# Optimization experiments

Hardware: AMD Instinct MI355X
Metric: run time of the kernel (lower is better)

## Reference

```python
import jax, jax.numpy as jnp
import numpy as np

B, V, H = 4, 256, 128
EPS = 1e-5


def setup_inputs() -> dict:
    key = jax.random.key(0)
    ks = jax.random.split(key, 16)
    s = 1.0 / np.sqrt(H)
    d = {}
    d["h"] = jax.random.normal(ks[0], (B, V, H), jnp.float32)
    d["e"] = jax.random.normal(ks[1], (B, V, V, H), jnp.float32)
    d["A"] = jax.random.bernoulli(ks[2], 0.5, (B, V, V))
    d["S"] = jax.random.bernoulli(ks[3], 0.5, (B, V, V))
    for i, n in enumerate("UVABC"):
        d["W" + n] = (jax.random.normal(ks[4 + i], (H, H), jnp.float32) * s)
        d["b" + n] = jnp.zeros((H,), jnp.float32)
    d["gamma_h"] = jnp.ones((H,), jnp.float32)
    d["beta_h"] = jnp.zeros((H,), jnp.float32)
    d["gamma_e"] = jnp.ones((H,), jnp.float32)
    d["beta_e"] = jnp.zeros((H,), jnp.float32)
    return d


def _batchnorm(x2d, gamma, beta):
    # BatchNorm1d with batch statistics (track_running_stats=False), biased var
    m = x2d.mean(axis=0)
    v = x2d.var(axis=0)
    return (x2d - m) * jax.lax.rsqrt(v + EPS) * gamma + beta


def reference(h, e, A, S, WU, bU, WV, bV, WA, bA, WB, bB, WC, bC,
              gamma_h, beta_h, gamma_e, beta_e):
    b, v, hd = h.shape
    h_in, e_in = h, e

    Uh = h @ WU.T + bU                      # (B,V,H)
    Vh = h @ WV.T + bV                      # (B,V,H)
    Ah = h @ WA.T + bA
    Bh = h @ WB.T + bB
    Ce = e @ WC.T + bC                      # (B,V,V,H)

    # e_new[b,i,j] = Ah[b,j] + Bh[b,i] + Ce[b,i,j]
    e_new = Ah[:, None, :, :] + Bh[:, :, None, :] + Ce
    gates = jax.nn.sigmoid(e_new)

    # aggregate(Vh, S, gates): zero where S is True, then sum over j
    Vh_b = Vh[:, None, :, :]                # (B,1,V,H) -> neighbor j features
    agg_S = jnp.sum(jnp.where(S[..., None], 0.0, gates * Vh_b), axis=2)
    # aggregate(Vh, A, gates=1): sum_j (1 - A[i,j]) * Vh[j] as a matmul
    agg_A = jnp.einsum('bij,bjh->bih', (~A).astype(Vh.dtype), Vh)

    h_new = Uh + agg_S + agg_A

    h_new = _batchnorm(h_new.reshape(b * v, hd), gamma_h, beta_h).reshape(b, v, hd)
    e_new = _batchnorm(e_new.reshape(b * v * v, hd), gamma_e, beta_e).reshape(b, v, v, hd)

    h_out = h_in + jax.nn.relu(h_new)
    e_out = e_in + jax.nn.relu(e_new)
    return (h_out, e_out)
```

## Files before the change

kernel.cpp:

```cpp
#include <hip/hip_runtime.h>

#define BB 4
#define VV 256
#define HH 128
#define NROWS (BB*VV)
#define NE_CNT (BB*VV*VV)
#define EPSV 1e-5f

typedef float4 f4;

__device__ __forceinline__ float sigm(float x) {
    return 1.f / (1.f + __expf(-x));
}

#define COMP(v,kk) ((kk)==0 ? (v).x : (kk)==1 ? (v).y : (kk)==2 ? (v).z : (v).w)

#define GLOAD_LDS16(g, l) __builtin_amdgcn_global_load_lds( \
    (const __attribute__((address_space(1))) unsigned int*)(g), \
    (__attribute__((address_space(3))) unsigned int*)(l), 16, 0, 0)

__global__ __launch_bounds__(256) void k_linear4(
    const float* __restrict__ h,
    const float* __restrict__ W0, const float* __restrict__ b0,
    const float* __restrict__ W1, const float* __restrict__ b1,
    const float* __restrict__ W2, const float* __restrict__ b2,
    const float* __restrict__ W3, const float* __restrict__ b3,
    float* __restrict__ out)
{
    __shared__ float hs[4*HH];
    const int tid = threadIdx.x;
    const int r0  = blockIdx.x * 4;
    if (tid < 128) {
        int r = tid >> 5, kq = (tid & 31) << 2;
        *(f4*)&hs[r*HH + kq] = *(const f4*)&h[(r0 + r)*HH + kq];
    }
    __syncthreads();
    const int n  = tid & 127;
    const int s0 = tid >> 7;
    const float* Ws[4] = {W0, W1, W2, W3};
    const float* bs[4] = {b0, b1, b2, b3};
    for (int ss = 0; ss < 2; ++ss) {
        const int sel = s0 + ss*2;
        const float* wrow = Ws[sel] + n*HH;
        float a0=0.f, a1=0.f, a2=0.f, a3=0.f;
        for (int kq = 0; kq < 32; ++kq) {
            f4 w = *(const f4*)&wrow[kq<<2];
            float wq[4] = {w.x, w.y, w.z, w.w};
            #pragma unroll
            for (int q = 0; q < 4; ++q) {
                int k = (kq<<2) + q;
                float wv = wq[q];
                a0 += hs[0*HH + k] * wv;
                a1 += hs[1*HH + k] * wv;
                a2 += hs[2*HH + k] * wv;
                a3 += hs[3*HH + k] * wv;
            }
        }
        float bias = bs[sel][n];
        float* o = out + sel*(NROWS*HH);
        o[(r0+0)*HH + n] = a0 + bias;
        o[(r0+1)*HH + n] = a1 + bias;
        o[(r0+2)*HH + n] = a2 + bias;
        o[(r0+3)*HH + n] = a3 + bias;
    }
}

__global__ __launch_bounds__(256) void k_transpose(
    const float* __restrict__ in, float* __restrict__ out)
{
    __shared__ float t[32][33];
    int ti = blockIdx.x >> 2, tj = blockIdx.x & 3;
    int tx = threadIdx.x & 31, ty = threadIdx.x >> 5;
    for (int yy = ty; yy < 32; yy += 8)
        t[yy][tx] = in[(ti*32 + yy)*HH + tj*32 + tx];
    __syncthreads();
    for (int yy = ty; yy < 32; yy += 8)
        out[(tj*32 + yy)*HH + ti*32 + tx] = t[tx][yy];
}

__global__ __launch_bounds__(256, 2) void k_edge(
    const float* __restrict__ e, const int* __restrict__ A, const int* __restrict__ S,
    const float* __restrict__ WCt, const float* __restrict__ bC,
    const float* __restrict__ Ahw, const float* __restrict__ Bhw,
    const float* __restrict__ Vhw,
    float* __restrict__ eout, float* __restrict__ aggS, float* __restrict__ aggA,
    float* __restrict__ sums)
{
    __shared__ float es[2][2048];
    __shared__ float wc[2][2048];
    __shared__ float s_aggS[HH], s_aggA[HH], s_sum[HH], s_ssq[HH];

    const int t     = threadIdx.x;
    const int bi    = blockIdx.x >> 1;
    const int jbase = (blockIdx.x & 1) << 7;
    const int b     = bi >> 8;
    if (t < HH) { s_aggS[t]=0.f; s_aggA[t]=0.f; s_sum[t]=0.f; s_ssq[t]=0.f; }

    const int tn  = t & 15;
    const int tjg = t >> 4;

    float acc[8][8];
    #pragma unroll
    for (int jj = 0; jj < 8; ++jj)
        #pragma unroll
        for (int q = 0; q < 8; ++q) acc[jj][q] = 0.f;

    const f4* e4   = (const f4*)e;
    const f4* wct4 = (const f4*)WCt;

    const int j0 = t >> 2;
    const int sp = (t & 3) ^ (j0 & 3);
    const f4* p_es0 = e4 + ((size_t)(bi*VV + jbase) + j0)*32 + sp;
    const f4* p_es1 = p_es0 + (size_t)64*32;
    const f4* p_wc  = wct4 + t;

    const int wave = t >> 6;
    const int wofs = wave * 256;

    #define STAGE(buf, kc_) do {                                        \
        float* esb_ = es[buf];                                          \
        float* wcb_ = wc[buf];                                          \
        GLOAD_LDS16(p_es0 + (kc_)*4,        &esb_[wofs]);               \
        GLOAD_LDS16(p_es1 + (kc_)*4,        &esb_[1024 + wofs]);        \
        GLOAD_LDS16(p_wc  + (kc_)*512,      &wcb_[wofs]);               \
        GLOAD_LDS16(p_wc  + (kc_)*512+256,  &wcb_[1024 + wofs]);        \
    } while (0)

    STAGE(0, 0);
    __syncthreads();

    for (int kc = 0; kc < 8; ++kc) {
        float* esb = es[kc & 1];
        float* wcb = wc[kc & 1];
        if (kc < 7) STAGE((kc & 1) ^ 1, kc + 1);
        #pragma unroll
        for (int kq = 0; kq < 4; ++kq) {
            const int sw = ((kq ^ (tjg & 3)) << 2);
            #pragma unroll
            for (int jh = 0; jh < 2; ++jh) {
                f4 a0 = *(const f4*)&esb[(tjg + (jh*4+0)*16)*16 + sw];
                f4 a1 = *(const f4*)&esb[(tjg + (jh*4+1)*16)*16 + sw];
                f4 a2 = *(const f4*)&esb[(tjg + (jh*4+2)*16)*16 + sw];
                f4 a3 = *(const f4*)&esb[(tjg + (jh*4+3)*16)*16 + sw];
                #pragma unroll
                for (int kk = 0; kk < 4; ++kk) {
                    const float* wrow = &wcb[(kq*4 + kk)*128 + tn*4];
                    f4 w0 = *(const f4*)&wrow[0];
                    f4 w1 = *(const f4*)&wrow[64];
                    float v0 = COMP(a0,kk), v1 = COMP(a1,kk);
                    float v2 = COMP(a2,kk), v3 = COMP(a3,kk);
                    #pragma unroll
                    for (int jl = 0; jl < 4; ++jl) {
                        float a = (jl==0)?v0:(jl==1)?v1:(jl==2)?v2:v3;
                        acc[jh*4+jl][0] += a*w0.x;
                        acc[jh*4+jl][1] += a*w0.y;
                        acc[jh*4+jl][2] += a*w0.z;
                        acc[jh*4+jl][3] += a*w0.w;
                        acc[jh*4+jl][4] += a*w1.x;
                        acc[jh*4+jl][5] += a*w1.y;
                        acc[jh*4+jl][6] += a*w1.z;
                        acc[jh*4+jl][7] += a*w1.w;
                    }
                }
            }
        }
        __syncthreads();
    }
    #undef STAGE

    float bcv[8], bhv[8];
    #pragma unroll
    for (int q = 0; q < 2; ++q) {
        f4 bc4 = *(const f4*)&bC[tn*4 + q*64];
        f4 bh4 = *(const f4*)&Bhw[bi*HH + tn*4 + q*64];
        bcv[q*4+0]=bc4.x; bcv[q*4+1]=bc4.y; bcv[q*4+2]=bc4.z; bcv[q*4+3]=bc4.w;
        bhv[q*4+0]=bh4.x; bhv[q*4+1]=bh4.y; bhv[q*4+2]=bh4.z; bhv[q*4+3]=bh4.w;
    }
    float sm[8], sq[8], aS[8], aA[8];
    #pragma unroll
    for (int q = 0; q < 8; ++q) { sm[q]=0.f; sq[q]=0.f; aS[q]=0.f; aA[q]=0.f; }

    const int* Sp = S + bi*VV + jbase;
    const int* Ap = A + bi*VV + jbase;
    #pragma unroll
    for (int jj = 0; jj < 8; ++jj) {
        const int j = tjg + jj*16;
        const int jg = jbase + j;
        const float* ahp = &Ahw[(size_t)(b*VV + jg)*HH];
        const float* vhp = &Vhw[(size_t)(b*VV + jg)*HH];
        const int Sij = Sp[j], Aij = Ap[j];
        #pragma unroll
        for (int q = 0; q < 2; ++q) {
            f4 ah = *(const f4*)&ahp[tn*4 + q*64];
            f4 vh = *(const f4*)&vhp[tn*4 + q*64];
            f4 env;
            env.x = acc[jj][q*4+0] + bcv[q*4+0] + bhv[q*4+0] + ah.x;
            env.y = acc[jj][q*4+1] + bcv[q*4+1] + bhv[q*4+1] + ah.y;
            env.z = acc[jj][q*4+2] + bcv[q*4+2] + bhv[q*4+2] + ah.z;
            env.w = acc[jj][q*4+3] + bcv[q*4+3] + bhv[q*4+3] + ah.w;
            *(f4*)&eout[((size_t)(bi*VV) + jg)*HH + tn*4 + q*64] = env;
            float vv[4] = {vh.x, vh.y, vh.z, vh.w};
            float ev[4] = {env.x, env.y, env.z, env.w};
            #pragma unroll
            for (int qq = 0; qq < 4; ++qq) {
                float v = ev[qq];
                sm[q*4+qq] += v;
                sq[q*4+qq] += v*v;
                if (!Aij) aA[q*4+qq] += vv[qq];
                if (!Sij) aS[q*4+qq] += vv[qq] * sigm(v);
            }
        }
    }
    #pragma unroll
    for (int q = 0; q < 2; ++q)
        #pragma unroll
        for (int qq = 0; qq < 4; ++qq) {
            int n = tn*4 + q*64 + qq;
            atomicAdd(&s_sum[n],  sm[q*4+qq]);
            atomicAdd(&s_ssq[n],  sq[q*4+qq]);
            atomicAdd(&s_aggS[n], aS[q*4+qq]);
            atomicAdd(&s_aggA[n], aA[q*4+qq]);
        }
    __syncthreads();
    if (t < HH) {
        atomicAdd(&aggS[bi*HH + t], s_aggS[t]);
        atomicAdd(&aggA[bi*HH + t], s_aggA[t]);
        atomicAdd(&sums[t],      s_sum[t]);
        atomicAdd(&sums[HH + t], s_ssq[t]);
    }
}

__global__ __launch_bounds__(256) void k_hnew(
    const float* __restrict__ Uh, const float* __restrict__ aggS,
    const float* __restrict__ aggA, float* __restrict__ h_new,
    float* __restrict__ sums)
{
    __shared__ float ssm[HH], ssq[HH];
    const int tid = threadIdx.x;
    if (tid < 128) { ssm[tid]=0.f; ssq[tid]=0.f; }
    __syncthreads();
    int gid = blockIdx.x*256 + tid;
    f4 u = *(const f4*)&Uh[gid*4];
    f4 s = *(const f4*)&aggS[gid*4];
    f4 a = *(const f4*)&aggA[gid*4];
    float v0=u.x+s.x+a.x, v1=u.y+s.y+a.y, v2=u.z+s.z+a.z, v3=u.w+s.w+a.w;
    *(f4*)&h_new[gid*4] = make_float4(v0,v1,v2,v3);
    int n0 = (gid*4) & 127;
    atomicAdd(&ssm[n0+0], v0); atomicAdd(&ssq[n0+0], v0*v0);
    atomicAdd(&ssm[n0+1], v1); atomicAdd(&ssq[n0+1], v1*v1);
    atomicAdd(&ssm[n0+2], v2); atomicAdd(&ssq[n0+2], v2*v2);
    atomicAdd(&ssm[n0+3], v3); atomicAdd(&ssq[n0+3], v3*v3);
    __syncthreads();
    if (tid < 128) {
        atomicAdd(&sums[256 + tid], ssm[tid]);
        atomicAdd(&sums[384 + tid], ssq[tid]);
    }
}

__global__ void k_stats(const float* __restrict__ sums, float* __restrict__ outs,
                        const float* __restrict__ gamma_e, const float* __restrict__ beta_e,
                        const float* __restrict__ gamma_h, const float* __restrict__ beta_h)
{
    int n = threadIdx.x;
    float em  = sums[n] * (1.f/(float)NE_CNT);
    float ev  = sums[128+n] * (1.f/(float)NE_CNT) - em*em;
    float esc = rsqrtf(ev + EPSV) * gamma_e[n];
    outs[n]       = esc;
    outs[128 + n] = beta_e[n] - em*esc;
    float hm  = sums[256+n] * (1.f/1024.f);
    float hv  = sums[384+n] * (1.f/1024.f) - hm*hm;
    float hsc = rsqrtf(hv + EPSV) * gamma_h[n];
    outs[256 + n] = hsc;
    outs[384 + n] = beta_h[n] - hm*hsc;
}

__global__ __launch_bounds__(256) void k_hout(
    const float* __restrict__ h_in, const float* __restrict__ h_new,
    const float* __restrict__ outs, float* __restrict__ hout)
{
    int gid = blockIdx.x*256 + threadIdx.x;
    int n0 = (gid*4) & 127;
    f4 x  = *(const f4*)&h_new[gid*4];
    f4 hi = *(const f4*)&h_in[gid*4];
    f4 sc = *(const f4*)&outs[256 + n0];
    f4 sh = *(const f4*)&outs[384 + n0];
    f4 y;
    y.x = fmaxf(x.x*sc.x + sh.x, 0.f) + hi.x;
    y.y = fmaxf(x.y*sc.y + sh.y, 0.f) + hi.y;
    y.z = fmaxf(x.z*sc.z + sh.z, 0.f) + hi.z;
    y.w = fmaxf(x.w*sc.w + sh.w, 0.f) + hi.w;
    *(f4*)&hout[gid*4] = y;
}

__global__ __launch_bounds__(256) void k_eout(
    const float* __restrict__ e_in, const float* __restrict__ outs,
    float* __restrict__ eio)
{
    size_t gid = (size_t)blockIdx.x*256 + threadIdx.x;
    int n0 = ((int)(gid & 31)) << 2;
    f4 x  = *(const f4*)&eio[gid*4];
    f4 ei = *(const f4*)&e_in[gid*4];
    f4 sc = *(const f4*)&outs[n0];
    f4 sh = *(const f4*)&outs[128 + n0];
    f4 y;
    y.x = fmaxf(x.x*sc.x + sh.x, 0.f) + ei.x;
    y.y = fmaxf(x.y*sc.y + sh.y, 0.f) + ei.y;
    y.z = fmaxf(x.z*sc.z + sh.z, 0.f) + ei.z;
    y.w = fmaxf(x.w*sc.w + sh.w, 0.f) + ei.w;
    *(f4*)&eio[gid*4] = y;
}

extern "C" void kernel_launch(void* const* d_in, const int* in_sizes, int n_in,
                              void* d_out, int out_size, void* d_ws, size_t ws_size,
                              hipStream_t stream)
{
    (void)in_sizes; (void)n_in; (void)out_size; (void)ws_size;
    const float* h   = (const float*)d_in[0];
    const float* e   = (const float*)d_in[1];
    const int*   A   = (const int*)d_in[2];
    const int*   S   = (const int*)d_in[3];
    const float* WU  = (const float*)d_in[4];   const float* bU = (const float*)d_in[5];
    const float* WV  = (const float*)d_in[6];   const float* bV = (const float*)d_in[7];
    const float* WA_ = (const float*)d_in[8];   const float* bA = (const float*)d_in[9];
    const float* WB_ = (const float*)d_in[10];  const float* bB = (const float*)d_in[11];
    const float* WC_ = (const float*)d_in[12];  const float* bC = (const float*)d_in[13];
    const float* gamma_h = (const float*)d_in[14]; const float* beta_h = (const float*)d_in[15];
    const float* gamma_e = (const float*)d_in[16]; const float* beta_e = (const float*)d_in[17];

    float* ws    = (float*)d_ws;
    float* Uh    = ws;
    float* Vh    = ws + 131072;
    float* Ahw   = ws + 262144;
    float* Bhw   = ws + 393216;
    float* aggS  = ws + 524288;
    float* aggA  = ws + 655360;
    float* h_new = ws + 786432;
    float* WCt   = ws + 917504;
    float* sums  = ws + 933888;
    float* outs  = ws + 934400;

    float* hout = (float*)d_out;
    float* eout = (float*)d_out + NROWS*HH;

    hipMemsetAsync(sums, 0, 512*sizeof(float), stream);
    hipMemsetAsync(aggS, 0, 262144*sizeof(float), stream);
    k_linear4 <<<256,   256, 0, stream>>>(h, WU,bU, WV,bV, WA_,bA, WB_,bB, Uh);
    k_transpose<<<16,   256, 0, stream>>>(WC_, WCt);
    k_edge    <<<2048,  256, 0, stream>>>(e, A, S, WCt, bC, Ahw, Bhw, Vh,
                                          eout, aggS, aggA, sums);
    k_hnew    <<<128,   256, 0, stream>>>(Uh, aggS, aggA, h_new, sums);
    k_stats   <<<1,     128, 0, stream>>>(sums, outs, gamma_e, beta_e, gamma_h, beta_h);
    k_hout    <<<128,   256, 0, stream>>>(h, h_new, outs, hout);
    k_eout    <<<32768, 256, 0, stream>>>(e, outs, eout);
}
```

Measured before the change: 510.8 us.

## Preload full WC into LDS and read edge features directly from global

```diff
diff --git a/kernel.cpp b/kernel.cpp
--- a/kernel.cpp
+++ b/kernel.cpp
@@ -86,87 +86,61 @@
     float* __restrict__ eout, float* __restrict__ aggS, float* __restrict__ aggA,
     float* __restrict__ sums)
 {
-    __shared__ float es[2][2048];
-    __shared__ float wc[2][2048];
-    __shared__ float s_aggS[HH], s_aggA[HH], s_sum[HH], s_ssq[HH];
+    __shared__ float wcs[HH*HH];
 
     const int t     = threadIdx.x;
     const int bi    = blockIdx.x >> 1;
     const int jbase = (blockIdx.x & 1) << 7;
     const int b     = bi >> 8;
-    if (t < HH) { s_aggS[t]=0.f; s_aggA[t]=0.f; s_sum[t]=0.f; s_ssq[t]=0.f; }
 
     const int tn  = t & 15;
     const int tjg = t >> 4;
 
+    {
+        const f4* wct4 = (const f4*)WCt;
+        const int wave = t >> 6;
+        #pragma unroll
+        for (int r = 0; r < 16; ++r)
+            GLOAD_LDS16(wct4 + r*256 + t, &wcs[r*1024 + wave*256]);
+    }
+    __syncthreads();
+
     float acc[8][8];
     #pragma unroll
-    for (int jj = 0; jj < 8; ++jj)
-        #pragma unroll
-        for (int q = 0; q < 8; ++q) acc[jj][q] = 0.f;
-
-    const f4* e4   = (const f4*)e;
-    const f4* wct4 = (const f4*)WCt;
-
-    const int j0 = t >> 2;
-    const int sp = (t & 3) ^ (j0 & 3);
-    const f4* p_es0 = e4 + ((size_t)(bi*VV + jbase) + j0)*32 + sp;
-    const f4* p_es1 = p_es0 + (size_t)64*32;
-    const f4* p_wc  = wct4 + t;
-
-    const int wave = t >> 6;
-    const int wofs = wave * 256;
-
-    #define STAGE(buf, kc_) do {                                        \
-        float* esb_ = es[buf];                                          \
-        float* wcb_ = wc[buf];                                          \
-        GLOAD_LDS16(p_es0 + (kc_)*4,        &esb_[wofs]);               \
-        GLOAD_LDS16(p_es1 + (kc_)*4,        &esb_[1024 + wofs]);        \
-        GLOAD_LDS16(p_wc  + (kc_)*512,      &wcb_[wofs]);               \
-        GLOAD_LDS16(p_wc  + (kc_)*512+256,  &wcb_[1024 + wofs]);        \
-    } while (0)
-
-    STAGE(0, 0);
-    __syncthreads();
-
-    for (int kc = 0; kc < 8; ++kc) {
-        float* esb = es[kc & 1];
-        float* wcb = wc[kc & 1];
-        if (kc < 7) STAGE((kc & 1) ^ 1, kc + 1);
-        #pragma unroll
-        for (int kq = 0; kq < 4; ++kq) {
-            const int sw = ((kq ^ (tjg & 3)) << 2);
+    for (int m = 0; m < 8; ++m)
+        #pragma unroll
+        for (int q = 0; q < 8; ++q) acc[m][q] = 0.f;
+
+    const f4* erow = (const f4*)e + (size_t)(bi*VV + jbase)*32;
+
+    for (int ks = 0; ks < 32; ++ks) {
+        f4 aj[8];
+        #pragma unroll
+        for (int m = 0; m < 8; ++m)
+            aj[m] = erow[(size_t)(tjg + m*16)*32 + ks];
+        #pragma unroll
+        for (int kk = 0; kk < 4; ++kk) {
+            const float* wrow = &wcs[(ks*4 + kk)*128 + tn*4];
+            f4 w0 = *(const f4*)&wrow[0];
+            f4 w1 = *(const f4*)&wrow[64];
             #pragma unroll
-            for (int jh = 0; jh < 2; ++jh) {
-                f4 a0 = *(const f4*)&esb[(tjg + (jh*4+0)*16)*16 + sw];
-                f4 a1 = *(const f4*)&esb[(tjg + (jh*4+1)*16)*16 + sw];
-                f4 a2 = *(const f4*)&esb[(tjg + (jh*4+2)*16)*16 + sw];
-                f4 a3 = *(const f4*)&esb[(tjg + (jh*4+3)*16)*16 + sw];
-                #pragma unroll
-                for (int kk = 0; kk < 4; ++kk) {
-                    const float* wrow = &wcb[(kq*4 + kk)*128 + tn*4];
-                    f4 w0 = *(const f4*)&wrow[0];
-                    f4 w1 = *(const f4*)&wrow[64];
-                    float v0 = COMP(a0,kk), v1 = COMP(a1,kk);
-                    float v2 = COMP(a2,kk), v3 = COMP(a3,kk);
-                    #pragma unroll
-                    for (int jl = 0; jl < 4; ++jl) {
-                        float a = (jl==0)?v0:(jl==1)?v1:(jl==2)?v2:v3;
-                        acc[jh*4+jl][0] += a*w0.x;
-                        acc[jh*4+jl][1] += a*w0.y;
-                        acc[jh*4+jl][2] += a*w0.z;
-                        acc[jh*4+jl][3] += a*w0.w;
-                        acc[jh*4+jl][4] += a*w1.x;
-                        acc[jh*4+jl][5] += a*w1.y;
-                        acc[jh*4+jl][6] += a*w1.z;
-                        acc[jh*4+jl][7] += a*w1.w;
-                    }
-                }
+            for (int m = 0; m < 8; ++m) {
+                float a = COMP(aj[m], kk);
+                acc[m][0] += a*w0.x; acc[m][1] += a*w0.y;
+                acc[m][2] += a*w0.z; acc[m][3] += a*w0.w;
+                acc[m][4] += a*w1.x; acc[m][5] += a*w1.y;
+                acc[m][6] += a*w1.z; acc[m][7] += a*w1.w;
             }
         }
-        __syncthreads();
-    }
-    #undef STAGE
+    }
+
+    __syncthreads();
+    float* s_aggS = wcs;
+    float* s_aggA = wcs + 128;
+    float* s_sum  = wcs + 256;
+    float* s_ssq  = wcs + 384;
+    if (t < HH) { s_aggS[t]=0.f; s_aggA[t]=0.f; s_sum[t]=0.f; s_ssq[t]=0.f; }
+    __syncthreads();
 
     float bcv[8], bhv[8];
     #pragma unroll
```

Measured after the change: 533.1 us. +4.4%, slower.
